# Kernel tuning notes

Measured on AMD Instinct MI355X. Metric: run time of the kernel, lower is better.

The kernel has to match this reference:

```python
import jax, jax.numpy as jnp
import numpy as np

SMPL_PARENTS = [-1, 0, 0, 0, 1, 2, 3, 4, 5, 6, 7, 8, 9, 9, 9, 12, 13, 14, 16, 17, 18, 19, 20, 21]
J = 24          # SMPL_NR_JOINTS
HID = 32        # hidden_dim
LSTM_H = HID * J  # 768

# Static skeleton adjacency incl. self loops (PyG GATConv add_self_loops=True).
# Edge (parent v -> child u): messages flow src=v to dst=u. adj[dst, src] = True.
_adj = np.eye(J, dtype=bool)
for u, v in enumerate(SMPL_PARENTS):
    if v >= 0:
        _adj[u, v] = True
ADJ = jnp.asarray(_adj)


def setup_inputs() -> dict:
    key = jax.random.key(0)
    ks = jax.random.split(key, 12)
    N, L = 128, 256
    s = lambda k, shp, scale: (jax.random.normal(k, shp, dtype=jnp.float32) * scale)
    return {
        "src": s(ks[0], (N, L, J * 3), 1.0),
        # pre: Linear(3 -> 32) + tanh
        "W_pre": s(ks[1], (3, HID), 0.3),
        "b_pre": s(ks[2], (HID,), 0.05),
        # GATConv(32 -> 32, heads=1): lin (no bias), att_src, att_dst, out bias
        "W_gat": s(ks[3], (HID, HID), 0.15),
        "att_src": s(ks[4], (HID,), 0.15),
        "att_dst": s(ks[5], (HID,), 0.15),
        "b_gat": s(ks[6], (HID,), 0.05),
        # LSTM(768 -> 768), gate order i, f, g, o (torch convention)
        "W_ih": s(ks[7], (4 * LSTM_H, LSTM_H), 0.02),
        "W_hh": s(ks[8], (4 * LSTM_H, LSTM_H), 0.02),
        "b_ih": s(ks[9], (4 * LSTM_H,), 0.02),
        "b_hh": s(ks[10], (4 * LSTM_H,), 0.02),
    }


def _gat_lstm(src, W_pre, b_pre, W_gat, att_src, att_dst, b_gat, W_ih, W_hh, b_ih, b_hh):
    N, L, D = src.shape
    A = D // J
    x = src.reshape(N * L, J, A)                       # [B, J, 3]
    x = jnp.tanh(x @ W_pre + b_pre)                    # pre: [B, J, H]

    # GATConv (heads=1, concat): vectorized over B copies of the static skeleton.
    xp = x @ W_gat                                     # [B, J, H]
    a_s = xp @ att_src                                 # [B, J] source term
    a_d = xp @ att_dst                                 # [B, J] dest term
    # e[b, i, j] = LeakyReLU(a_d[i] + a_s[j]) for edge j -> i (incl. self loops)
    e = jax.nn.leaky_relu(a_d[:, :, None] + a_s[:, None, :], negative_slope=0.2)
    e = jnp.where(ADJ[None, :, :], e, -jnp.inf)
    attn = jax.nn.softmax(e, axis=-1)                  # softmax over incoming edges
    g = jnp.einsum('bij,bjh->bih', attn, xp) + b_gat   # [B, J, H]

    X = g.reshape(N, L, J * HID)                       # from_graph_seq -> [N, L, 768]

    # LSTM (num_layers=1, batch_first), torch gate order i, f, g, o
    def step(carry, x_t):
        h, c = carry
        gates = x_t @ W_ih.T + b_ih + h @ W_hh.T + b_hh  # [N, 4*768]
        i_g, f_g, g_g, o_g = jnp.split(gates, 4, axis=-1)
        c = jax.nn.sigmoid(f_g) * c + jax.nn.sigmoid(i_g) * jnp.tanh(g_g)
        h = jax.nn.sigmoid(o_g) * jnp.tanh(c)
        return (h, c), h

    h0 = jnp.zeros((N, LSTM_H), dtype=X.dtype)
    (h_n, c_n), ys = jax.lax.scan(step, (h0, h0), X.transpose(1, 0, 2))
    output = ys.transpose(1, 0, 2)                     # [N, L, 768]
    return output, h_n[None], c_n[None]                # (out, (h_n, c_n)) like nn.LSTM


def reference(src, W_pre, b_pre, W_gat, att_src, att_dst, b_gat, W_ih, W_hh, b_ih, b_hh):
    return _gat_lstm(src, W_pre, b_pre, W_gat, att_src, att_dst, b_gat, W_ih, W_hh, b_ih, b_hh)
```

## Files before the change

kernel.cpp:

```cpp
#include <hip/hip_runtime.h>
#include <hip/hip_bf16.h>


#define NB 128
#define LSEQ 256
#define LH 768
#define BGR 32768
#define NWG 96
#define PWG 192

typedef __attribute__((ext_vector_type(8))) short short8;
typedef __attribute__((ext_vector_type(4))) float floatx4;
typedef __attribute__((ext_vector_type(4))) unsigned int uint4v;
typedef __attribute__((ext_vector_type(2))) unsigned int uint2v;

union frag16 { uint4v u; short8 s; };
union bfbits { __hip_bfloat16 h; unsigned short s; };
union uf2 { uint2v u; float f[2]; };

__device__ __forceinline__ float fsig(float x) {
    return __builtin_amdgcn_rcpf(1.f + __builtin_amdgcn_exp2f(-1.44269504f * x));
}
__device__ __forceinline__ float ftanhf(float x) {
    return 1.f - 2.f * __builtin_amdgcn_rcpf(1.f + __builtin_amdgcn_exp2f(2.88539008f * x));
}

__device__ __forceinline__ float bf16bits_to_f(unsigned short s) {
    unsigned u = ((unsigned)s) << 16;
    float f;
    __builtin_memcpy(&f, &u, 4);
    return f;
}

__device__ __forceinline__ void issue8(uint4v* b, const char* base) {
    asm volatile("global_load_dwordx4 %0, %1, off sc0 sc1"            : "=v"(b[0]) : "v"(base));
    asm volatile("global_load_dwordx4 %0, %1, off offset:64 sc0 sc1"  : "=v"(b[1]) : "v"(base));
    asm volatile("global_load_dwordx4 %0, %1, off offset:128 sc0 sc1" : "=v"(b[2]) : "v"(base));
    asm volatile("global_load_dwordx4 %0, %1, off offset:192 sc0 sc1" : "=v"(b[3]) : "v"(base));
    asm volatile("global_load_dwordx4 %0, %1, off offset:256 sc0 sc1" : "=v"(b[4]) : "v"(base));
    asm volatile("global_load_dwordx4 %0, %1, off offset:320 sc0 sc1" : "=v"(b[5]) : "v"(base));
    asm volatile("global_load_dwordx4 %0, %1, off offset:384 sc0 sc1" : "=v"(b[6]) : "v"(base));
    asm volatile("global_load_dwordx4 %0, %1, off offset:448 sc0 sc1" : "=v"(b[7]) : "v"(base));
}
__device__ __forceinline__ void issueG2(uint2v* g, const char* gb) {
    const char* gb2 = gb + 6144;
    asm volatile("global_load_dwordx2 %0, %1, off"             : "=v"(g[0]) : "v"(gb));
    asm volatile("global_load_dwordx2 %0, %1, off offset:3072" : "=v"(g[1]) : "v"(gb));
    asm volatile("global_load_dwordx2 %0, %1, off"             : "=v"(g[2]) : "v"(gb2));
    asm volatile("global_load_dwordx2 %0, %1, off offset:3072" : "=v"(g[3]) : "v"(gb2));
}
__device__ __forceinline__ void wait8g_touch(uint4v* b, uint2v* g) {
    asm volatile("s_waitcnt vmcnt(8)"
        : "+v"(b[0]), "+v"(b[1]), "+v"(b[2]), "+v"(b[3]),
          "+v"(b[4]), "+v"(b[5]), "+v"(b[6]), "+v"(b[7]),
          "+v"(g[0]), "+v"(g[1]), "+v"(g[2]), "+v"(g[3]) :: "memory");
}
__device__ __forceinline__ void wait8_touch(uint4v* b) {
    asm volatile("s_waitcnt vmcnt(8)"
        : "+v"(b[0]), "+v"(b[1]), "+v"(b[2]), "+v"(b[3]),
          "+v"(b[4]), "+v"(b[5]), "+v"(b[6]), "+v"(b[7]) :: "memory");
}
__device__ __forceinline__ void wait0_touch(uint4v* b) {
    asm volatile("s_waitcnt vmcnt(0)"
        : "+v"(b[0]), "+v"(b[1]), "+v"(b[2]), "+v"(b[3]),
          "+v"(b[4]), "+v"(b[5]), "+v"(b[6]), "+v"(b[7]) :: "memory");
}

__global__ __launch_bounds__(256) void convert_kernel(
    const float* W_pre, const float* b_pre, const float* W_gat,
    const float* att_src, const float* att_dst, const float* b_gat,
    const float* W_ih, const float* W_hh, const float* b_ih, const float* b_hh,
    __hip_bfloat16* __restrict__ WihC, __hip_bfloat16* __restrict__ WhhC,
    float* __restrict__ smallC)
{
    long i = (long)blockIdx.x * 256 + threadIdx.x;
    if (i < 2359296) { WihC[i] = __float2bfloat16(W_ih[i]); return; }
    i -= 2359296;
    if (i < 2359296) { WhhC[i] = __float2bfloat16(W_hh[i]); return; }
    i -= 2359296;
    if (i < 96)   { smallC[0 + i]    = W_pre[i];   return; }  i -= 96;
    if (i < 32)   { smallC[96 + i]   = b_pre[i];   return; }  i -= 32;
    if (i < 1024) { smallC[128 + i]  = W_gat[i];   return; }  i -= 1024;
    if (i < 32)   { smallC[1152 + i] = att_src[i]; return; }  i -= 32;
    if (i < 32)   { smallC[1184 + i] = att_dst[i]; return; }  i -= 32;
    if (i < 32)   { smallC[1216 + i] = b_gat[i];   return; }  i -= 32;
    if (i < 3072) { smallC[1248 + i] = b_ih[i];    return; }  i -= 3072;
    if (i < 3072) { smallC[4320 + i] = b_hh[i];    return; }
}

__global__ __launch_bounds__(256) void gat_pre_kernel(
    const float* __restrict__ src,
    const float* __restrict__ smallC,
    __hip_bfloat16* __restrict__ Xb)
{
    __shared__ float wpre[96];
    __shared__ float bpre[32];
    __shared__ float wgat[1024];
    __shared__ float asrc[32];
    __shared__ float adst[32];
    __shared__ float bgat[32];
    __shared__ float xl[8][72];
    __shared__ float hl[8][24][32];
    __shared__ float xpl[8][24][32];
    __shared__ float asl[8][24];
    __shared__ float adl[8][24];

    const int tid = threadIdx.x;
    for (int i = tid; i < 96; i += 256)   wpre[i] = smallC[i];
    for (int i = tid; i < 1024; i += 256) wgat[i] = smallC[128 + i];
    if (tid < 32) {
        bpre[tid] = smallC[96 + tid];
        asrc[tid] = smallC[1152 + tid];
        adst[tid] = smallC[1184 + tid];
        bgat[tid] = smallC[1216 + tid];
    }

    const int g = tid >> 5;
    const int k = tid & 31;
    const long gb = (long)blockIdx.x * 8 + g;

    for (int i = k; i < 72; i += 32)
        xl[g][i] = src[gb * 72 + i];
    __syncthreads();

    #pragma unroll
    for (int j = 0; j < 24; ++j) {
        float v = xl[g][j*3+0] * wpre[0*32+k]
                + xl[g][j*3+1] * wpre[1*32+k]
                + xl[g][j*3+2] * wpre[2*32+k] + bpre[k];
        hl[g][j][k] = tanhf(v);
    }
    __syncthreads();

    #pragma unroll
    for (int j = 0; j < 24; ++j) {
        float v = 0.f;
        #pragma unroll
        for (int m = 0; m < 32; ++m) v += hl[g][j][m] * wgat[m*32 + k];
        xpl[g][j][k] = v;
    }
    __syncthreads();

    if (k < 24) {
        float vs = 0.f, vd = 0.f;
        #pragma unroll
        for (int m = 0; m < 32; ++m) {
            float x = xpl[g][k][m];
            vs += x * asrc[m];
            vd += x * adst[m];
        }
        asl[g][k] = vs;
        adl[g][k] = vd;
    }
    __syncthreads();

    const int par[24] = {-1,0,0,0,1,2,3,4,5,6,7,8,9,9,9,12,13,14,16,17,18,19,20,21};
    #pragma unroll
    for (int j = 0; j < 24; ++j) {
        int p = par[j];
        float o;
        if (p < 0) {
            o = xpl[g][j][k] + bgat[k];
        } else {
            float es = adl[g][j] + asl[g][j];
            float ep = adl[g][j] + asl[g][p];
            es = es > 0.f ? es : 0.2f * es;
            ep = ep > 0.f ? ep : 0.2f * ep;
            float mx = fmaxf(es, ep);
            float wse = expf(es - mx), wpe = expf(ep - mx);
            float inv = 1.f / (wse + wpe);
            o = (wse * xpl[g][j][k] + wpe * xpl[g][p][k]) * inv + bgat[k];
        }
        Xb[gb * 768 + j * 32 + k] = __float2bfloat16(o);
    }
}

__global__ __launch_bounds__(256) void gates_in_kernel(
    const __hip_bfloat16* __restrict__ Xb,
    const __hip_bfloat16* __restrict__ Wih,
    const float* __restrict__ smallC,
    float* __restrict__ Gf, __hip_bfloat16* __restrict__ Gb, int ginf)
{
    const int tid = threadIdx.x;
    const int w = tid >> 6, L = tid & 63;
    const int rh2 = w >> 1, ch2 = w & 1;
    const int q = L >> 4, col16 = L & 15;
    const int R0 = blockIdx.x * 128;
    const int N0 = blockIdx.y * 128;

    const short8* ap[4];
    const short8* bp[4];
    #pragma unroll
    for (int i = 0; i < 4; ++i) {
        ap[i] = (const short8*)(Xb + (size_t)(R0 + 64*rh2 + 16*i + col16) * 768 + q*8);
        bp[i] = (const short8*)(Wih + (size_t)(N0 + 64*ch2 + 16*i + col16) * 768 + q*8);
    }

    floatx4 acc[4][4] = {};
    for (int kk = 0; kk < 24; ++kk) {
        short8 a[4], b[4];
        #pragma unroll
        for (int i = 0; i < 4; ++i) { a[i] = ap[i][kk*4]; b[i] = bp[i][kk*4]; }
        #pragma unroll
        for (int rt = 0; rt < 4; ++rt)
            #pragma unroll
            for (int bt = 0; bt < 4; ++bt)
                acc[rt][bt] = __builtin_amdgcn_mfma_f32_16x16x32_bf16(a[rt], b[bt], acc[rt][bt], 0, 0, 0);
    }

    #pragma unroll
    for (int bt = 0; bt < 4; ++bt) {
        int wrow = N0 + 64*ch2 + 16*bt + col16;
        float bias = smallC[1248 + wrow] + smallC[4320 + wrow];
        #pragma unroll
        for (int rt = 0; rt < 4; ++rt) {
            #pragma unroll
            for (int r = 0; r < 4; ++r) {
                int m_abs = R0 + 64*rh2 + 16*rt + q*4 + r;
                int mm = m_abs >> 8, tt = m_abs & 255;
                size_t idx = ((size_t)tt * 128 + mm) * 3072 + wrow;
                float v = acc[rt][bt][r] + bias;
                if (ginf) Gf[idx] = v;
                else      Gb[idx] = __float2bfloat16(v);
            }
        }
    }
}

__global__ __launch_bounds__(256) void lstm_persist_kernel(
    const void* __restrict__ Gin,
    const __hip_bfloat16* __restrict__ Whh,
    __hip_bfloat16* __restrict__ h0g,
    __hip_bfloat16* __restrict__ h1g,
    float* __restrict__ out,
    int* __restrict__ bar,
    int* __restrict__ barU,
    int ginf)
{
    __shared__ short8 whhs[3072];
    __shared__ float gl[64 * 33];

    const int tid = threadIdx.x;
    const int w = tid >> 6;
    const int L = tid & 63;
    const int q = L >> 4;
    const int col16 = L & 15;
    const int cg = blockIdx.x % 96;
    const int rg = blockIdx.x / 96;

    for (int b = 0; b < 12; ++b) {
        int f = tid + 256 * b;
        int kk = f >> 7, c = (f >> 2) & 31, qq = f & 3;
        int wrow = 768 * (c >> 3) + cg * 8 + (c & 7);
        whhs[f] = *(const short8*)(Whh + (size_t)wrow * 768 + kk * 32 + qq * 8);
    }
    __syncthreads();

    const int m_loc = tid >> 2;
    const int u2b = (tid & 3) * 2;
    const int m_glob = rg * 64 + m_loc;
    float creg0 = 0.f, creg1 = 0.f;

    const float* Gf = (const float*)Gin;
    const __hip_bfloat16* Gb = (const __hip_bfloat16*)Gin;
    const size_t gcol = cg * 8 + u2b;

    uint2v gp[4] = {};
    if (ginf)
        issueG2(gp, (const char*)(Gf + (size_t)m_glob * 3072 + gcol));

    for (int t = 0; t < LSEQ; ++t) {
        const char* hr = (const char*)((t & 1) ? h1g : h0g);
        __hip_bfloat16* hw = (t & 1) ? h0g : h1g;

        floatx4 acc0 = {}, acc1 = {};
        uint4v bufA[8], bufB[8];
        const char* hbase = hr + (size_t)(((rg * 64 + 16 * w + col16) * 768) + q * 8) * 2;

        issue8(bufA, hbase);
        issue8(bufB, hbase + 512);

        wait8g_touch(bufA, gp);
        #pragma unroll
        for (int j = 0; j < 8; ++j) {
            frag16 fu; fu.u = bufA[j];
            short8 bv0 = whhs[j * 128 + (col16 * 4 + q)];
            short8 bv1 = whhs[j * 128 + ((16 + col16) * 4 + q)];
            acc0 = __builtin_amdgcn_mfma_f32_16x16x32_bf16(fu.s, bv0, acc0, 0, 0, 0);
            acc1 = __builtin_amdgcn_mfma_f32_16x16x32_bf16(fu.s, bv1, acc1, 0, 0, 0);
        }
        issue8(bufA, hbase + 1024);
        wait8_touch(bufB);
        #pragma unroll
        for (int j = 0; j < 8; ++j) {
            frag16 fu; fu.u = bufB[j];
            short8 bv0 = whhs[(8 + j) * 128 + (col16 * 4 + q)];
            short8 bv1 = whhs[(8 + j) * 128 + ((16 + col16) * 4 + q)];
            acc0 = __builtin_amdgcn_mfma_f32_16x16x32_bf16(fu.s, bv0, acc0, 0, 0, 0);
            acc1 = __builtin_amdgcn_mfma_f32_16x16x32_bf16(fu.s, bv1, acc1, 0, 0, 0);
        }
        wait0_touch(bufA);
        #pragma unroll
        for (int j = 0; j < 8; ++j) {
            frag16 fu; fu.u = bufA[j];
            short8 bv0 = whhs[(16 + j) * 128 + (col16 * 4 + q)];
            short8 bv1 = whhs[(16 + j) * 128 + ((16 + col16) * 4 + q)];
            acc0 = __builtin_amdgcn_mfma_f32_16x16x32_bf16(fu.s, bv0, acc0, 0, 0, 0);
            acc1 = __builtin_amdgcn_mfma_f32_16x16x32_bf16(fu.s, bv1, acc1, 0, 0, 0);
        }

        #pragma unroll
        for (int r = 0; r < 4; ++r) {
            int mr = 16 * w + q * 4 + r;
            gl[mr * 33 + col16] = acc0[r];
            gl[mr * 33 + 16 + col16] = acc1[r];
        }
        __syncthreads();

        float gI0, gI1, gF0, gF1, gG0, gG1, gO0, gO1;
        if (ginf) {
            uf2 uI, uF, uG, uO;
            uI.u = gp[0]; uF.u = gp[1]; uG.u = gp[2]; uO.u = gp[3];
            gI0 = uI.f[0]; gI1 = uI.f[1]; gF0 = uF.f[0]; gF1 = uF.f[1];
            gG0 = uG.f[0]; gG1 = uG.f[1]; gO0 = uO.f[0]; gO1 = uO.f[1];
        } else {
            const size_t grow = ((size_t)t * 128 + m_glob) * 3072 + gcol;
            unsigned vi = *(const unsigned*)(Gb + grow);
            unsigned vf = *(const unsigned*)(Gb + grow + 768);
            unsigned vg = *(const unsigned*)(Gb + grow + 1536);
            unsigned vo = *(const unsigned*)(Gb + grow + 2304);
            gI0 = bf16bits_to_f(vi & 0xFFFF); gI1 = bf16bits_to_f(vi >> 16);
            gF0 = bf16bits_to_f(vf & 0xFFFF); gF1 = bf16bits_to_f(vf >> 16);
            gG0 = bf16bits_to_f(vg & 0xFFFF); gG1 = bf16bits_to_f(vg >> 16);
            gO0 = bf16bits_to_f(vo & 0xFFFF); gO1 = bf16bits_to_f(vo >> 16);
        }

        float ig0 = gI0 + gl[m_loc * 33 + 0  + u2b];
        float fg0 = gF0 + gl[m_loc * 33 + 8  + u2b];
        float gg0 = gG0 + gl[m_loc * 33 + 16 + u2b];
        float og0 = gO0 + gl[m_loc * 33 + 24 + u2b];
        float ig1 = gI1 + gl[m_loc * 33 + 0  + u2b + 1];
        float fg1 = gF1 + gl[m_loc * 33 + 8  + u2b + 1];
        float gg1 = gG1 + gl[m_loc * 33 + 16 + u2b + 1];
        float og1 = gO1 + gl[m_loc * 33 + 24 + u2b + 1];

        float si0 = fsig(ig0), sf0 = fsig(fg0), so0 = fsig(og0);
        float cn0 = sf0 * creg0 + si0 * ftanhf(gg0);
        float hv0 = so0 * ftanhf(cn0);
        creg0 = cn0;
        float si1 = fsig(ig1), sf1 = fsig(fg1), so1 = fsig(og1);
        float cn1 = sf1 * creg1 + si1 * ftanhf(gg1);
        float hv1 = so1 * ftanhf(cn1);
        creg1 = cn1;

        bfbits b0, b1;
        b0.h = __float2bfloat16(hv0);
        b1.h = __float2bfloat16(hv1);
        unsigned hpack = (unsigned)b0.s | ((unsigned)b1.s << 16);
        char* ha = (char*)hw + (size_t)(m_glob * 768 + cg * 8 + u2b) * 2;
        float2 ov; ov.x = hv0; ov.y = hv1;
        float* oa = out + ((size_t)m_glob * 256 + t) * 768 + cg * 8 + u2b;

        if (t < LSEQ - 1) {
            asm volatile("global_store_dword %0, %1, off sc0 sc1" :: "v"(ha), "v"(hpack) : "memory");
            asm volatile("global_store_dwordx2 %0, %1, off" :: "v"(oa), "v"(ov) : "memory");
            if (ginf)
                issueG2(gp, (const char*)(Gf + ((size_t)(t + 1) * 128 + m_glob) * 3072 + gcol));
            asm volatile("s_waitcnt vmcnt(5)" ::: "memory");
            __builtin_amdgcn_s_barrier();
            if (tid == 0) {
                int g = blockIdx.x & 7;
                int prev = __hip_atomic_fetch_add(&barU[(t * 10 + g) * 32], 1,
                                                  __ATOMIC_RELAXED, __HIP_MEMORY_SCOPE_AGENT);
                bool rel = false;
                if (prev == 23) {
                    int pr = __hip_atomic_fetch_add(&barU[(t * 10 + 8) * 32], 1,
                                                    __ATOMIC_RELAXED, __HIP_MEMORY_SCOPE_AGENT);
                    if (pr == 7) {
                        __hip_atomic_store(&bar[2040], t + 1,
                                           __ATOMIC_RELAXED, __HIP_MEMORY_SCOPE_AGENT);
                        rel = true;
                    }
                }
                if (!rel) {
                    while (__hip_atomic_load(&bar[2040], __ATOMIC_RELAXED,
                                             __HIP_MEMORY_SCOPE_AGENT) < t + 1)
                        __builtin_amdgcn_s_sleep(2);
                }
            }
            __builtin_amdgcn_s_barrier();
        } else {
            asm volatile("global_store_dwordx2 %0, %1, off" :: "v"(oa), "v"(ov) : "memory");
            const size_t base = (size_t)NB * LSEQ * LH;
            const size_t ci = (size_t)m_glob * 768 + cg * 8 + u2b;
            float2 hv; hv.x = hv0; hv.y = hv1;
            float2 cv; cv.x = cn0; cv.y = cn1;
            *(float2*)(out + base + ci) = hv;
            *(float2*)(out + base + (size_t)NB * LH + ci) = cv;
        }
    }
}

__global__ __launch_bounds__(256) void lstm_step_kernel(
    const __hip_bfloat16* __restrict__ Xb,
    const __hip_bfloat16* __restrict__ Wih,
    const __hip_bfloat16* __restrict__ Whh,
    const float* __restrict__ smallC,
    float* __restrict__ cst,
    const __hip_bfloat16* __restrict__ hr,
    __hip_bfloat16* __restrict__ hw,
    float* __restrict__ out,
    int t)
{
    __shared__ float gls[128 * 33];
    const int tid = threadIdx.x;
    const int w = tid >> 6;
    const int L = tid & 63;
    const int rh = w >> 1;
    const int ct = w & 1;
    const int q = L >> 4;
    const int col16 = L & 15;
    const int c_local = 16 * ct + col16;
    const int gate = c_local >> 3;
    const int uu = c_local & 7;
    const int u = 8 * blockIdx.x + uu;
    const int wrow = 768 * gate + u;

    const short8* bp_i = (const short8*)(Wih + (long)wrow * 768 + q * 8);
    const short8* bp_h = (const short8*)(Whh + (long)wrow * 768 + q * 8);
    const short8* ap_x[4];
    const short8* ap_h[4];
    #pragma unroll
    for (int rt = 0; rt < 4; ++rt) {
        int m = 64 * rh + 16 * rt + col16;
        ap_x[rt] = (const short8*)(Xb + ((long)m * LSEQ + t) * 768 + q * 8);
        ap_h[rt] = (const short8*)(hr + (long)m * 768 + q * 8);
    }
    floatx4 acc[4] = {};
    for (int kk = 0; kk < 768; kk += 32) {
        short8 bv = bp_i[kk >> 3];
        #pragma unroll
        for (int rt = 0; rt < 4; ++rt)
            acc[rt] = __builtin_amdgcn_mfma_f32_16x16x32_bf16(ap_x[rt][kk >> 3], bv, acc[rt], 0, 0, 0);
    }
    for (int kk = 0; kk < 768; kk += 32) {
        short8 bv = bp_h[kk >> 3];
        #pragma unroll
        for (int rt = 0; rt < 4; ++rt)
            acc[rt] = __builtin_amdgcn_mfma_f32_16x16x32_bf16(ap_h[rt][kk >> 3], bv, acc[rt], 0, 0, 0);
    }
    float bias = smallC[1248 + wrow] + smallC[4320 + wrow];
    #pragma unroll
    for (int rt = 0; rt < 4; ++rt)
        #pragma unroll
        for (int r = 0; r < 4; ++r) {
            int m = 64 * rh + 16 * rt + q * 4 + r;
            gls[m * 33 + c_local] = acc[rt][r] + bias;
        }
    __syncthreads();
    for (int item = tid; item < 1024; item += 256) {
        int m = item >> 3;
        int u2l = item & 7;
        float ig = gls[m * 33 + 0  + u2l];
        float fg = gls[m * 33 + 8  + u2l];
        float gg = gls[m * 33 + 16 + u2l];
        float og = gls[m * 33 + 24 + u2l];
        int u2 = 8 * blockIdx.x + u2l;
        int ci = m * 768 + u2;
        float co = cst[ci];
        float si = 1.f / (1.f + expf(-ig));
        float sf = 1.f / (1.f + expf(-fg));
        float so = 1.f / (1.f + expf(-og));
        float cn = sf * co + si * tanhf(gg);
        float h = so * tanhf(cn);
        cst[ci] = cn;
        hw[ci] = __float2bfloat16(h);
        out[((long)m * LSEQ + t) * 768 + u2] = h;
    }
}

__global__ __launch_bounds__(256) void finalize_kernel(
    const __hip_bfloat16* __restrict__ hfin,
    const float* __restrict__ cst,
    float* __restrict__ out)
{
    int i = blockIdx.x * 256 + threadIdx.x;
    const long base = (long)NB * LSEQ * LH;
    out[base + i] = __bfloat162float(hfin[i]);
    out[base + NB * LH + i] = cst[i];
}

extern "C" void kernel_launch(void* const* d_in, const int* in_sizes, int n_in,
                              void* d_out, int out_size, void* d_ws, size_t ws_size,
                              hipStream_t stream) {
    const float* src     = (const float*)d_in[0];
    const float* W_pre   = (const float*)d_in[1];
    const float* b_pre   = (const float*)d_in[2];
    const float* W_gat   = (const float*)d_in[3];
    const float* att_src = (const float*)d_in[4];
    const float* att_dst = (const float*)d_in[5];
    const float* b_gat   = (const float*)d_in[6];
    const float* W_ih    = (const float*)d_in[7];
    const float* W_hh    = (const float*)d_in[8];
    const float* b_ih    = (const float*)d_in[9];
    const float* b_hh    = (const float*)d_in[10];

    float* out = (float*)d_out;
    char* ws = (char*)d_ws;

    __hip_bfloat16* Xb     = (__hip_bfloat16*)(ws);
    __hip_bfloat16* WihC   = (__hip_bfloat16*)(ws + 50331648);
    __hip_bfloat16* WhhC   = (__hip_bfloat16*)(ws + 55050240);
    float*          cs     = (float*)         (ws + 59768832);
    __hip_bfloat16* h0     = (__hip_bfloat16*)(ws + 60162048);
    __hip_bfloat16* h1     = (__hip_bfloat16*)(ws + 60358656);
    float*          smallC = (float*)         (ws + 60555264);
    int*            bar    = (int*)           (ws + 60588032);
    void*           Gin    = (void*)          (ws + 60596224);

    const size_t base_need = 60596224;
    const size_t need_f32  = base_need + (size_t)BGR * 3072 * 4;
    const size_t need_b16  = base_need + (size_t)BGR * 3072 * 2;
    const int use_persist  = (ws_size >= need_b16);
    const int ginf         = (ws_size >= need_f32);

    hipMemsetAsync(h0, 0, NB * LH * sizeof(__hip_bfloat16), stream);

    const long conv_total = 2359296L * 2 + 7392;
    convert_kernel<<<(int)((conv_total + 255) / 256), 256, 0, stream>>>(
        W_pre, b_pre, W_gat, att_src, att_dst, b_gat,
        W_ih, W_hh, b_ih, b_hh, WihC, WhhC, smallC);

    gat_pre_kernel<<<BGR / 8, 256, 0, stream>>>(src, smallC, Xb);

    if (use_persist) {
        hipMemsetAsync(bar, 0, 8192, stream);
        hipMemsetAsync(cs, 0, 327680, stream);
        dim3 ggrid(256, 24);
        gates_in_kernel<<<ggrid, 256, 0, stream>>>(Xb, WihC, smallC,
                                                   (float*)Gin, (__hip_bfloat16*)Gin, ginf);
        lstm_persist_kernel<<<PWG, 256, 0, stream>>>(Gin, WhhC, h0, h1, out,
                                                     bar, (int*)cs, ginf);
    } else {
        hipMemsetAsync(cs, 0, NB * LH * sizeof(float), stream);
        __hip_bfloat16* hp[2] = {h0, h1};
        for (int t = 0; t < LSEQ; ++t) {
            lstm_step_kernel<<<NWG, 256, 0, stream>>>(Xb, WihC, WhhC, smallC,
                                                      cs, hp[t & 1], hp[(t + 1) & 1],
                                                      out, t);
        }
        finalize_kernel<<<NB * LH / 256, 256, 0, stream>>>(h0, cs, out);
    }
}
```

Baseline: 2.509 ms.

## Scope grid barrier to row groups and prefetch all h loads up front

The persistent LSTM kernel's grid-wide barrier becomes a per-row-group barrier. Each row group of 96 workgroups only needs the h rows it produces itself, so it now syncs on its own monotonically increasing counters and epoch flag instead of a full-grid barrier. This removes a separate barrier buffer and its memset and reduces cross-group waiting. The step also issues all three h load batches before the first MFMA block, raising the vmcnt threshold, to overlap more memory latency at the cost of extra registers.

```diff
diff --git a/kernel.cpp b/kernel.cpp
--- a/kernel.cpp
+++ b/kernel.cpp
@@ -49,8 +49,8 @@
     asm volatile("global_load_dwordx2 %0, %1, off"             : "=v"(g[2]) : "v"(gb2));
     asm volatile("global_load_dwordx2 %0, %1, off offset:3072" : "=v"(g[3]) : "v"(gb2));
 }
-__device__ __forceinline__ void wait8g_touch(uint4v* b, uint2v* g) {
-    asm volatile("s_waitcnt vmcnt(8)"
+__device__ __forceinline__ void wait16g_touch(uint4v* b, uint2v* g) {
+    asm volatile("s_waitcnt vmcnt(16)"
         : "+v"(b[0]), "+v"(b[1]), "+v"(b[2]), "+v"(b[3]),
           "+v"(b[4]), "+v"(b[5]), "+v"(b[6]), "+v"(b[7]),
           "+v"(g[0]), "+v"(g[1]), "+v"(g[2]), "+v"(g[3]) :: "memory");
@@ -233,7 +233,6 @@
     __hip_bfloat16* __restrict__ h0g,
     __hip_bfloat16* __restrict__ h1g,
     float* __restrict__ out,
-    int* __restrict__ bar,
     int* __restrict__ barU,
     int ginf)
 {
@@ -265,6 +264,10 @@
     const __hip_bfloat16* Gb = (const __hip_bfloat16*)Gin;
     const size_t gcol = cg * 8 + u2b;
 
+    int* myL1    = &barU[(rg * 16 + (cg & 7)) * 32];
+    int* myL2    = &barU[(rg * 16 + 8) * 32];
+    int* myEpoch = &barU[(rg * 16 + 9) * 32];
+
     uint2v gp[4] = {};
     if (ginf)
         issueG2(gp, (const char*)(Gf + (size_t)m_glob * 3072 + gcol));
@@ -274,13 +277,14 @@
         __hip_bfloat16* hw = (t & 1) ? h0g : h1g;
 
         floatx4 acc0 = {}, acc1 = {};
-        uint4v bufA[8], bufB[8];
+        uint4v bufA[8], bufB[8], bufC[8];
         const char* hbase = hr + (size_t)(((rg * 64 + 16 * w + col16) * 768) + q * 8) * 2;
 
         issue8(bufA, hbase);
         issue8(bufB, hbase + 512);
-
-        wait8g_touch(bufA, gp);
+        issue8(bufC, hbase + 1024);
+
+        wait16g_touch(bufA, gp);
         #pragma unroll
         for (int j = 0; j < 8; ++j) {
             frag16 fu; fu.u = bufA[j];
@@ -289,7 +293,6 @@
             acc0 = __builtin_amdgcn_mfma_f32_16x16x32_bf16(fu.s, bv0, acc0, 0, 0, 0);
             acc1 = __builtin_amdgcn_mfma_f32_16x16x32_bf16(fu.s, bv1, acc1, 0, 0, 0);
         }
-        issue8(bufA, hbase + 1024);
         wait8_touch(bufB);
         #pragma unroll
         for (int j = 0; j < 8; ++j) {
@@ -299,10 +302,10 @@
             acc0 = __builtin_amdgcn_mfma_f32_16x16x32_bf16(fu.s, bv0, acc0, 0, 0, 0);
             acc1 = __builtin_amdgcn_mfma_f32_16x16x32_bf16(fu.s, bv1, acc1, 0, 0, 0);
         }
-        wait0_touch(bufA);
+        wait0_touch(bufC);
         #pragma unroll
         for (int j = 0; j < 8; ++j) {
-            frag16 fu; fu.u = bufA[j];
+            frag16 fu; fu.u = bufC[j];
             short8 bv0 = whhs[(16 + j) * 128 + (col16 * 4 + q)];
             short8 bv1 = whhs[(16 + j) * 128 + ((16 + col16) * 4 + q)];
             acc0 = __builtin_amdgcn_mfma_f32_16x16x32_bf16(fu.s, bv0, acc0, 0, 0, 0);
@@ -369,21 +372,20 @@
             asm volatile("s_waitcnt vmcnt(5)" ::: "memory");
             __builtin_amdgcn_s_barrier();
             if (tid == 0) {
-                int g = blockIdx.x & 7;
-                int prev = __hip_atomic_fetch_add(&barU[(t * 10 + g) * 32], 1,
+                int prev = __hip_atomic_fetch_add(myL1, 1,
                                                   __ATOMIC_RELAXED, __HIP_MEMORY_SCOPE_AGENT);
                 bool rel = false;
-                if (prev == 23) {
-                    int pr = __hip_atomic_fetch_add(&barU[(t * 10 + 8) * 32], 1,
+                if (prev == 12 * (t + 1) - 1) {
+                    int pr = __hip_atomic_fetch_add(myL2, 1,
                                                     __ATOMIC_RELAXED, __HIP_MEMORY_SCOPE_AGENT);
-                    if (pr == 7) {
-                        __hip_atomic_store(&bar[2040], t + 1,
+                    if (pr == 8 * (t + 1) - 1) {
+                        __hip_atomic_store(myEpoch, t + 1,
                                            __ATOMIC_RELAXED, __HIP_MEMORY_SCOPE_AGENT);
                         rel = true;
                     }
                 }
                 if (!rel) {
-                    while (__hip_atomic_load(&bar[2040], __ATOMIC_RELAXED,
+                    while (__hip_atomic_load(myEpoch, __ATOMIC_RELAXED,
                                              __HIP_MEMORY_SCOPE_AGENT) < t + 1)
                         __builtin_amdgcn_s_sleep(2);
                 }
@@ -515,7 +517,6 @@
     __hip_bfloat16* h0     = (__hip_bfloat16*)(ws + 60162048);
     __hip_bfloat16* h1     = (__hip_bfloat16*)(ws + 60358656);
     float*          smallC = (float*)         (ws + 60555264);
-    int*            bar    = (int*)           (ws + 60588032);
     void*           Gin    = (void*)          (ws + 60596224);
 
     const size_t base_need = 60596224;
@@ -534,13 +535,12 @@
     gat_pre_kernel<<<BGR / 8, 256, 0, stream>>>(src, smallC, Xb);
 
     if (use_persist) {
-        hipMemsetAsync(bar, 0, 8192, stream);
         hipMemsetAsync(cs, 0, 327680, stream);
         dim3 ggrid(256, 24);
         gates_in_kernel<<<ggrid, 256, 0, stream>>>(Xb, WihC, smallC,
                                                    (float*)Gin, (__hip_bfloat16*)Gin, ginf);
         lstm_persist_kernel<<<PWG, 256, 0, stream>>>(Gin, WhhC, h0, h1, out,
-                                                     bar, (int*)cs, ginf);
+                                                     (int*)cs, ginf);
     } else {
         hipMemsetAsync(cs, 0, NB * LH * sizeof(float), stream);
         __hip_bfloat16* hp[2] = {h0, h1};
```

Result: faster. 2.451 ms (-2.3%).
